# Performance work log

Hardware: AMD Instinct MI355X
Metric: run time of the kernel (lower is better)

The kernel has to match this reference:

```python
import jax, jax.numpy as jnp
import numpy as np

B, N, T, D = 8, 512, 64, 128
H = 8
DK = D // H
KS = 3
CAUSAL_PAD = KS - 1          # query conv: pad both sides, crop tail
SYM_PAD = (KS - 1) // 2      # key conv: 'same' padding


def setup_inputs() -> dict:
    key0 = jax.random.key(0)
    ks = jax.random.split(key0, 12)
    s = 0.05  # weight scale to keep activations in a sane range
    inp = {
        "query": jax.random.normal(ks[0], (B, N, T, D), jnp.float32),
        "key": jax.random.normal(ks[1], (B, N, T, D), jnp.float32),
        "value": jax.random.normal(ks[2], (B, N, T, D), jnp.float32),
        # causal mask (batch, T, T): 1 where attention allowed
        "mask": jnp.broadcast_to(jnp.tril(jnp.ones((T, T), jnp.int32)), (B, T, T)),
        "Wq": jax.random.normal(ks[3], (D, D, 1, KS), jnp.float32) * s,
        "bq": jax.random.normal(ks[4], (D,), jnp.float32) * s,
        "Wk": jax.random.normal(ks[5], (D, D, 1, KS), jnp.float32) * s,
        "bk": jax.random.normal(ks[6], (D,), jnp.float32) * s,
        "W0": jax.random.normal(ks[7], (D, D), jnp.float32) * s,
        "b0": jax.random.normal(ks[8], (D,), jnp.float32) * s,
        "W1": jax.random.normal(ks[9], (D, D), jnp.float32) * s,
        "b1": jax.random.normal(ks[10], (D,), jnp.float32) * s,
        "query_multi_segment": 0,
        "key_multi_segment": 1,
    }
    return inp


def _temporal_conv(x, W, b, pad):
    # x: (B, N, T, D) -> NCHW (B, D, N, T); W: (O, I, 1, K) OIHW
    xt = jnp.transpose(x, (0, 3, 1, 2))
    y = jax.lax.conv_general_dilated(
        xt, W, window_strides=(1, 1),
        padding=[(0, 0), (pad, pad)],
        dimension_numbers=("NCHW", "OIHW", "NCHW"))
    return y + b[None, :, None, None]  # (B, D, N, T')


def _to_heads(y_bdnt, nbatches):
    # (B, D, N, T) -> view (B, H, DK, N, T) -> permute -> (B, N, H, T, DK)
    Bb, Dd, Nn, Tt = y_bdnt.shape
    y = y_bdnt.reshape(Bb, H, DK, Nn, Tt)
    return jnp.transpose(y, (0, 3, 1, 4, 2))


def reference(query, key, value, mask, Wq, bq, Wk, bk, W0, b0, W1, b1,
              query_multi_segment, key_multi_segment):
    del query_multi_segment, key_multi_segment  # static: (False, True) branch, h_length == T
    nbatches = query.shape[0]

    # causal conv for query: pad (k-1) both sides, crop last (k-1)
    q = _temporal_conv(query, Wq, bq, CAUSAL_PAD)[:, :, :, :-CAUSAL_PAD]
    q = _to_heads(q, nbatches)                       # (B, N, H, T, DK)
    # 'same' conv for key
    k = _to_heads(_temporal_conv(key, Wk, bk, SYM_PAD), nbatches)  # (B, N, H, T, DK)

    # value linear: x @ W0.T + b0, then split heads
    v = jnp.einsum("bntd,ed->bnte", value, W0) + b0
    v = jnp.transpose(v.reshape(nbatches, N, T, H, DK), (0, 1, 3, 2, 4))  # (B, N, H, T, DK)

    scores = jnp.einsum("bnhqd,bnhkd->bnhqk", q, k) / jnp.sqrt(jnp.float32(DK))
    m = mask[:, None, None, :, :]                    # (B, 1, 1, T, T)
    scores = jnp.where(m == 0, jnp.float32(-1e9), scores)
    p_attn = jax.nn.softmax(scores, axis=-1)         # dropout p=0.0 -> identity

    x = jnp.einsum("bnhqk,bnhkd->bnhqd", p_attn, v)  # (B, N, H, T, DK)
    x = jnp.transpose(x, (0, 1, 3, 2, 4)).reshape(nbatches, N, T, H * DK)
    return jnp.einsum("bntd,ed->bnte", x, W1) + b1
```

## Files before the change

kernel.cpp:

```cpp
#include <hip/hip_runtime.h>
#include <hip/hip_bf16.h>
#include <stdint.h>
#include <math.h>

constexpr int Tt = 64;
constexpr int Dd = 128;
constexpr int BN = 4096;

typedef short s16x8 __attribute__((ext_vector_type(8)));
typedef short s16x4 __attribute__((ext_vector_type(4)));
typedef float f32x4 __attribute__((ext_vector_type(4)));

__device__ __forceinline__ short f2bf(float f) {
  return (short)__bfloat16_as_ushort(__float2bfloat16(f));
}

#define SQ_OFF   0
#define SK_OFF   16384
#define SV_OFF   32768
#define LDS_TOTAL 49152

__device__ __forceinline__ int swz256(int row, int colElem) {
  return (row << 8) + ((colElem << 1) ^ ((row & 7) << 4));
}
__device__ __forceinline__ int swz128(int row, int colElem) {
  return (row << 7) + ((colElem << 1) ^ ((row & 7) << 4));
}

__global__ void prep_weights(const float* __restrict__ Wq, const float* __restrict__ Wk,
                             const float* __restrict__ W0, const float* __restrict__ W1,
                             short* __restrict__ ws) {
  int i = blockIdx.x * 256 + threadIdx.x;
  if (i >= 131072) return;
  if (i < 49152) {
    int s = i >> 14, rem = i & 16383, o = rem >> 7, ii = rem & 127;
    ws[i] = f2bf(Wq[(o * 128 + ii) * 3 + s] * 0.36067376022224085f);
  } else if (i < 98304) {
    int j = i - 49152;
    int s = j >> 14, rem = j & 16383, o = rem >> 7, ii = rem & 127;
    ws[i] = f2bf(Wk[(o * 128 + ii) * 3 + s]);
  } else if (i < 114688) {
    ws[i] = f2bf(W0[i - 98304]);
  } else {
    ws[i] = f2bf(W1[i - 114688]);
  }
}

__launch_bounds__(512, 4)
__global__ void fused_attn(const float* __restrict__ query, const float* __restrict__ key,
                           const float* __restrict__ value, const short* __restrict__ wsb,
                           const float* __restrict__ bq, const float* __restrict__ bk,
                           const float* __restrict__ b0, const float* __restrict__ b1,
                           float* __restrict__ out) {
  __shared__ unsigned char smem[LDS_TOTAL];
  const int bn = blockIdx.x;
  const int tid = threadIdx.x;
  const int wave = tid >> 6;
  const int lane = tid & 63;
  const size_t base = (size_t)bn * (Tt * Dd);

  const int col = wave * 16 + (lane & 15);
  const int ke = 8 * (lane >> 4);
  const int arow = lane & 15;

  const short* wq = wsb;
  const short* wk = wsb + 49152;
  const short* wv = wsb + 98304;
  const short* w1 = wsb + 114688;

  {
    const int row0 = tid >> 5;
    const int c4 = (tid & 31) << 2;
#pragma unroll
    for (int t3 = 0; t3 < 3; ++t3) {
      const float* sp = (t3 == 0) ? query : (t3 == 1) ? key : value;
      const float4* s4 = (const float4*)(sp + base) + tid;
      const int a0 = ((t3 == 0) ? SQ_OFF : (t3 == 1) ? SK_OFF : SV_OFF) + swz256(row0, c4);
#pragma unroll
      for (int j = 0; j < 4; ++j) {
        float4 v = s4[j * 512];
        s16x4 b = {f2bf(v.x), f2bf(v.y), f2bf(v.z), f2bf(v.w)};
        *(s16x4*)(smem + a0 + j * 4096) = b;
      }
    }
  }
  const float bqv = bq[col] * 0.36067376022224085f;
  const float bkv = bk[col];
  const float b0v = b0[col];
  __syncthreads();

  f32x4 aq[4], ak[4], av[4];
#pragma unroll
  for (int rb = 0; rb < 4; ++rb) {
    aq[rb] = (f32x4){bqv, bqv, bqv, bqv};
    ak[rb] = (f32x4){bkv, bkv, bkv, bkv};
    av[rb] = (f32x4){b0v, b0v, b0v, b0v};
  }
#pragma unroll
  for (int kk = 0; kk < 4; ++kk) {
    s16x8 bvf = *(const s16x8*)(wv + (col << 7) + kk * 32 + ke);
#pragma unroll
    for (int rb = 0; rb < 4; ++rb) {
      s16x8 afv = *(const s16x8*)(smem + SV_OFF + swz256(rb * 16 + arow, kk * 32 + ke));
      av[rb] = __builtin_amdgcn_mfma_f32_16x16x32_bf16(afv, bvf, av[rb], 0, 0, 0);
    }
  }
#pragma unroll
  for (int s = 0; s < 3; ++s) {
#pragma unroll
    for (int kk = 0; kk < 4; ++kk) {
      s16x8 bqf = *(const s16x8*)(wq + (s << 14) + (col << 7) + kk * 32 + ke);
      s16x8 bkf = *(const s16x8*)(wk + (s << 14) + (col << 7) + kk * 32 + ke);
#pragma unroll
      for (int rb = 0; rb < 4; ++rb) {
        const int trq = rb * 16 + arow + s - 2;
        s16x8 afq = (s16x8){0, 0, 0, 0, 0, 0, 0, 0};
        if (rb == 0 && s < 2) {
          if (trq >= 0) afq = *(const s16x8*)(smem + SQ_OFF + swz256(trq, kk * 32 + ke));
        } else {
          afq = *(const s16x8*)(smem + SQ_OFF + swz256(trq, kk * 32 + ke));
        }
        aq[rb] = __builtin_amdgcn_mfma_f32_16x16x32_bf16(afq, bqf, aq[rb], 0, 0, 0);
        const int trk = rb * 16 + arow + s - 1;
        s16x8 afk = (s16x8){0, 0, 0, 0, 0, 0, 0, 0};
        if (rb == 0 && s == 0) {
          if (trk >= 0) afk = *(const s16x8*)(smem + SK_OFF + swz256(trk, kk * 32 + ke));
        } else if (rb == 3 && s == 2) {
          if (trk <= 63) afk = *(const s16x8*)(smem + SK_OFF + swz256(trk, kk * 32 + ke));
        } else {
          afk = *(const s16x8*)(smem + SK_OFF + swz256(trk, kk * 32 + ke));
        }
        ak[rb] = __builtin_amdgcn_mfma_f32_16x16x32_bf16(afk, bkf, ak[rb], 0, 0, 0);
      }
    }
  }
  __syncthreads();

#pragma unroll
  for (int rb = 0; rb < 4; ++rb)
#pragma unroll
    for (int r = 0; r < 4; ++r) {
      const int row = rb * 16 + (lane >> 4) * 4 + r;
      *(short*)(smem + SQ_OFF + swz256(row, col)) = f2bf(aq[rb][r]);
      *(short*)(smem + SK_OFF + swz256(row, col)) = f2bf(ak[rb][r]);
      *(short*)(smem + SV_OFF + swz128(col, row)) = f2bf(av[rb][r]);
    }
  __syncthreads();

  {
    const int g = lane >> 4;
    const int qrow = lane & 15;
#pragma unroll
    for (int j = 0; j < 4; ++j) {
      const int h = (wave + j) & 7;
      const int rb = 3 - j;
      s16x8 bfq = *(const s16x8*)(smem + SQ_OFF + swz256(rb * 16 + qrow, h * 16 + ke));
      f32x4 sacc[4];
#pragma unroll
      for (int c = 0; c <= rb; ++c) {
        s16x8 af = (s16x8){0, 0, 0, 0, 0, 0, 0, 0};
        if (lane < 32)
          af = *(const s16x8*)(smem + SK_OFF + swz256(c * 16 + qrow, h * 16 + ke));
        sacc[c] = __builtin_amdgcn_mfma_f32_16x16x32_bf16(
            af, bfq, (f32x4){0.f, 0.f, 0.f, 0.f}, 0, 0, 0);
      }
      float mx = -3.0e38f;
#pragma unroll
      for (int c = 0; c < rb; ++c)
#pragma unroll
        for (int r = 0; r < 4; ++r) mx = fmaxf(mx, sacc[c][r]);
#pragma unroll
      for (int r = 0; r < 4; ++r) {
        float sv = (4 * g + r <= qrow) ? sacc[rb][r] : -3.0e38f;
        sacc[rb][r] = sv;
        mx = fmaxf(mx, sv);
      }
      mx = fmaxf(mx, __shfl_xor(mx, 16));
      mx = fmaxf(mx, __shfl_xor(mx, 32));
      float sm = 0.f;
#pragma unroll
      for (int c = 0; c <= rb; ++c)
#pragma unroll
        for (int r = 0; r < 4; ++r) {
          float e = exp2f(sacc[c][r] - mx);
          sacc[c][r] = e;
          sm += e;
        }
      sm += __shfl_xor(sm, 16);
      sm += __shfl_xor(sm, 32);
      const float inv = 1.0f / sm;
      f32x4 xacc = (f32x4){0.f, 0.f, 0.f, 0.f};
#pragma unroll
      for (int c = 0; c <= rb; ++c) {
        s16x4 pa;
#pragma unroll
        for (int r = 0; r < 4; ++r) pa[r] = f2bf(sacc[c][r] * inv);
        s16x4 vf = *(const s16x4*)(smem + SV_OFF + swz128(h * 16 + qrow, c * 16 + 4 * g));
        xacc = __builtin_amdgcn_mfma_f32_16x16x16bf16_1k(pa, vf, xacc, 0, 0, 0);
      }
#pragma unroll
      for (int r = 0; r < 4; ++r)
        *(short*)(smem + SQ_OFF + swz256(rb * 16 + 4 * g + r, h * 16 + qrow)) = f2bf(xacc[r]);
    }
  }
  const float bv = b1[col];
  __syncthreads();

  {
    f32x4 acc[4];
#pragma unroll
    for (int rb = 0; rb < 4; ++rb) acc[rb] = (f32x4){bv, bv, bv, bv};
#pragma unroll
    for (int kk = 0; kk < 4; ++kk) {
      s16x8 bf = *(const s16x8*)(w1 + (col << 7) + kk * 32 + ke);
#pragma unroll
      for (int rb = 0; rb < 4; ++rb) {
        s16x8 af = *(const s16x8*)(smem + SQ_OFF + swz256(rb * 16 + arow, kk * 32 + ke));
        acc[rb] = __builtin_amdgcn_mfma_f32_16x16x32_bf16(af, bf, acc[rb], 0, 0, 0);
      }
    }
#pragma unroll
    for (int rb = 0; rb < 4; ++rb)
#pragma unroll
      for (int r = 0; r < 4; ++r) {
        const int row = rb * 16 + (lane >> 4) * 4 + r;
        out[base + (size_t)row * Dd + col] = acc[rb][r];
      }
  }
}

extern "C" void kernel_launch(void* const* d_in, const int* in_sizes, int n_in,
                              void* d_out, int out_size, void* d_ws, size_t ws_size,
                              hipStream_t stream) {
  (void)in_sizes; (void)n_in; (void)out_size; (void)ws_size;
  const float* query = (const float*)d_in[0];
  const float* key   = (const float*)d_in[1];
  const float* value = (const float*)d_in[2];
  const float* Wq = (const float*)d_in[4];
  const float* bq = (const float*)d_in[5];
  const float* Wk = (const float*)d_in[6];
  const float* bk = (const float*)d_in[7];
  const float* W0 = (const float*)d_in[8];
  const float* b0 = (const float*)d_in[9];
  const float* W1 = (const float*)d_in[10];
  const float* b1 = (const float*)d_in[11];
  float* out = (float*)d_out;
  short* wsb = (short*)d_ws;

  hipLaunchKernelGGL(prep_weights, dim3(512), dim3(256), 0, stream, Wq, Wk, W0, W1, wsb);
  hipLaunchKernelGGL(fused_attn, dim3(BN), dim3(512), 0, stream,
                     query, key, value, wsb, bq, bk, b0, b1, out);
}
```

Baseline: 210.1 us.

## Swap MFMA operand order so accumulators hold contiguous features for vector stores

The weight and activation operands of the projection and output MFMAs are swapped, so each lane's accumulator holds four consecutive feature columns of one time row. Results can then go to LDS as 8-byte packed stores and to global memory as 16-byte float4 stores, where the old code wrote scattered 2-byte and 4-byte elements. The PV MFMA is also transposed, and softmax normalization moves from every probability to the final output row. Biases are loaded as float4. This changes fragment layouts across several stages, so any indexing mistake would corrupt results, and LDS bank conflicts may shift.

Result: slower. 217.3 us (+3.4%).

```diff
diff --git a/kernel.cpp b/kernel.cpp
--- a/kernel.cpp
+++ b/kernel.cpp
@@ -59,9 +59,10 @@
   const int lane = tid & 63;
   const size_t base = (size_t)bn * (Tt * Dd);
 
-  const int col = wave * 16 + (lane & 15);
+  const int arow = lane & 15;
   const int ke = 8 * (lane >> 4);
-  const int arow = lane & 15;
+  const int d4 = wave * 16 + (lane >> 4) * 4;
+  const int wrow = wave * 16 + arow;
 
   const short* wq = wsb;
   const short* wk = wsb + 49152;
@@ -84,21 +85,22 @@
       }
     }
   }
-  const float bqv = bq[col] * 0.36067376022224085f;
-  const float bkv = bk[col];
-  const float b0v = b0[col];
-  __syncthreads();
-
+  const float4 bq4 = *(const float4*)(bq + d4);
+  const float4 bk4 = *(const float4*)(bk + d4);
+  const float b0v = b0[wave * 16 + arow];
+  __syncthreads();
+
+  constexpr float LS = 0.36067376022224085f;
   f32x4 aq[4], ak[4], av[4];
 #pragma unroll
-  for (int rb = 0; rb < 4; ++rb) {
-    aq[rb] = (f32x4){bqv, bqv, bqv, bqv};
-    ak[rb] = (f32x4){bkv, bkv, bkv, bkv};
-    av[rb] = (f32x4){b0v, b0v, b0v, b0v};
+  for (int tb = 0; tb < 4; ++tb) {
+    aq[tb] = (f32x4){bq4.x * LS, bq4.y * LS, bq4.z * LS, bq4.w * LS};
+    ak[tb] = (f32x4){bk4.x, bk4.y, bk4.z, bk4.w};
+    av[tb] = (f32x4){b0v, b0v, b0v, b0v};
   }
 #pragma unroll
   for (int kk = 0; kk < 4; ++kk) {
-    s16x8 bvf = *(const s16x8*)(wv + (col << 7) + kk * 32 + ke);
+    s16x8 bvf = *(const s16x8*)(wv + (wrow << 7) + kk * 32 + ke);
 #pragma unroll
     for (int rb = 0; rb < 4; ++rb) {
       s16x8 afv = *(const s16x8*)(smem + SV_OFF + swz256(rb * 16 + arow, kk * 32 + ke));
@@ -109,42 +111,43 @@
   for (int s = 0; s < 3; ++s) {
 #pragma unroll
     for (int kk = 0; kk < 4; ++kk) {
-      s16x8 bqf = *(const s16x8*)(wq + (s << 14) + (col << 7) + kk * 32 + ke);
-      s16x8 bkf = *(const s16x8*)(wk + (s << 14) + (col << 7) + kk * 32 + ke);
-#pragma unroll
-      for (int rb = 0; rb < 4; ++rb) {
-        const int trq = rb * 16 + arow + s - 2;
-        s16x8 afq = (s16x8){0, 0, 0, 0, 0, 0, 0, 0};
-        if (rb == 0 && s < 2) {
-          if (trq >= 0) afq = *(const s16x8*)(smem + SQ_OFF + swz256(trq, kk * 32 + ke));
+      s16x8 wqf = *(const s16x8*)(wq + (s << 14) + (wrow << 7) + kk * 32 + ke);
+      s16x8 wkf = *(const s16x8*)(wk + (s << 14) + (wrow << 7) + kk * 32 + ke);
+#pragma unroll
+      for (int tb = 0; tb < 4; ++tb) {
+        const int trq = tb * 16 + arow + s - 2;
+        s16x8 xq = (s16x8){0, 0, 0, 0, 0, 0, 0, 0};
+        if (tb == 0 && s < 2) {
+          if (trq >= 0) xq = *(const s16x8*)(smem + SQ_OFF + swz256(trq, kk * 32 + ke));
         } else {
-          afq = *(const s16x8*)(smem + SQ_OFF + swz256(trq, kk * 32 + ke));
+          xq = *(const s16x8*)(smem + SQ_OFF + swz256(trq, kk * 32 + ke));
         }
-        aq[rb] = __builtin_amdgcn_mfma_f32_16x16x32_bf16(afq, bqf, aq[rb], 0, 0, 0);
-        const int trk = rb * 16 + arow + s - 1;
-        s16x8 afk = (s16x8){0, 0, 0, 0, 0, 0, 0, 0};
-        if (rb == 0 && s == 0) {
-          if (trk >= 0) afk = *(const s16x8*)(smem + SK_OFF + swz256(trk, kk * 32 + ke));
-        } else if (rb == 3 && s == 2) {
-          if (trk <= 63) afk = *(const s16x8*)(smem + SK_OFF + swz256(trk, kk * 32 + ke));
+        aq[tb] = __builtin_amdgcn_mfma_f32_16x16x32_bf16(wqf, xq, aq[tb], 0, 0, 0);
+        const int trk = tb * 16 + arow + s - 1;
+        s16x8 xk = (s16x8){0, 0, 0, 0, 0, 0, 0, 0};
+        if (tb == 0 && s == 0) {
+          if (trk >= 0) xk = *(const s16x8*)(smem + SK_OFF + swz256(trk, kk * 32 + ke));
+        } else if (tb == 3 && s == 2) {
+          if (trk <= 63) xk = *(const s16x8*)(smem + SK_OFF + swz256(trk, kk * 32 + ke));
         } else {
-          afk = *(const s16x8*)(smem + SK_OFF + swz256(trk, kk * 32 + ke));
+          xk = *(const s16x8*)(smem + SK_OFF + swz256(trk, kk * 32 + ke));
         }
-        ak[rb] = __builtin_amdgcn_mfma_f32_16x16x32_bf16(afk, bkf, ak[rb], 0, 0, 0);
-      }
-    }
-  }
-  __syncthreads();
-
-#pragma unroll
-  for (int rb = 0; rb < 4; ++rb)
-#pragma unroll
-    for (int r = 0; r < 4; ++r) {
-      const int row = rb * 16 + (lane >> 4) * 4 + r;
-      *(short*)(smem + SQ_OFF + swz256(row, col)) = f2bf(aq[rb][r]);
-      *(short*)(smem + SK_OFF + swz256(row, col)) = f2bf(ak[rb][r]);
-      *(short*)(smem + SV_OFF + swz128(col, row)) = f2bf(av[rb][r]);
-    }
+        ak[tb] = __builtin_amdgcn_mfma_f32_16x16x32_bf16(wkf, xk, ak[tb], 0, 0, 0);
+      }
+    }
+  }
+  __syncthreads();
+
+#pragma unroll
+  for (int tb = 0; tb < 4; ++tb) {
+    const int t = tb * 16 + arow;
+    s16x4 pq = {f2bf(aq[tb][0]), f2bf(aq[tb][1]), f2bf(aq[tb][2]), f2bf(aq[tb][3])};
+    *(s16x4*)(smem + SQ_OFF + swz256(t, d4)) = pq;
+    s16x4 pk = {f2bf(ak[tb][0]), f2bf(ak[tb][1]), f2bf(ak[tb][2]), f2bf(ak[tb][3])};
+    *(s16x4*)(smem + SK_OFF + swz256(t, d4)) = pk;
+    s16x4 pv = {f2bf(av[tb][0]), f2bf(av[tb][1]), f2bf(av[tb][2]), f2bf(av[tb][3])};
+    *(s16x4*)(smem + SV_OFF + swz128(wave * 16 + arow, tb * 16 + (lane >> 4) * 4)) = pv;
+  }
   __syncthreads();
 
   {
@@ -194,38 +197,36 @@
       for (int c = 0; c <= rb; ++c) {
         s16x4 pa;
 #pragma unroll
-        for (int r = 0; r < 4; ++r) pa[r] = f2bf(sacc[c][r] * inv);
+        for (int r = 0; r < 4; ++r) pa[r] = f2bf(sacc[c][r]);
         s16x4 vf = *(const s16x4*)(smem + SV_OFF + swz128(h * 16 + qrow, c * 16 + 4 * g));
-        xacc = __builtin_amdgcn_mfma_f32_16x16x16bf16_1k(pa, vf, xacc, 0, 0, 0);
-      }
-#pragma unroll
-      for (int r = 0; r < 4; ++r)
-        *(short*)(smem + SQ_OFF + swz256(rb * 16 + 4 * g + r, h * 16 + qrow)) = f2bf(xacc[r]);
-    }
-  }
-  const float bv = b1[col];
+        xacc = __builtin_amdgcn_mfma_f32_16x16x16bf16_1k(vf, pa, xacc, 0, 0, 0);
+      }
+      s16x4 px = {f2bf(xacc[0] * inv), f2bf(xacc[1] * inv),
+                  f2bf(xacc[2] * inv), f2bf(xacc[3] * inv)};
+      *(s16x4*)(smem + SQ_OFF + swz256(rb * 16 + qrow, h * 16 + 4 * g)) = px;
+    }
+  }
+  const float4 b14 = *(const float4*)(b1 + d4);
   __syncthreads();
 
   {
-    f32x4 acc[4];
-#pragma unroll
-    for (int rb = 0; rb < 4; ++rb) acc[rb] = (f32x4){bv, bv, bv, bv};
+    f32x4 oacc[4];
+#pragma unroll
+    for (int tb = 0; tb < 4; ++tb) oacc[tb] = (f32x4){b14.x, b14.y, b14.z, b14.w};
 #pragma unroll
     for (int kk = 0; kk < 4; ++kk) {
-      s16x8 bf = *(const s16x8*)(w1 + (col << 7) + kk * 32 + ke);
-#pragma unroll
-      for (int rb = 0; rb < 4; ++rb) {
-        s16x8 af = *(const s16x8*)(smem + SQ_OFF + swz256(rb * 16 + arow, kk * 32 + ke));
-        acc[rb] = __builtin_amdgcn_mfma_f32_16x16x32_bf16(af, bf, acc[rb], 0, 0, 0);
-      }
-    }
-#pragma unroll
-    for (int rb = 0; rb < 4; ++rb)
-#pragma unroll
-      for (int r = 0; r < 4; ++r) {
-        const int row = rb * 16 + (lane >> 4) * 4 + r;
-        out[base + (size_t)row * Dd + col] = acc[rb][r];
-      }
+      s16x8 w1f = *(const s16x8*)(w1 + (wrow << 7) + kk * 32 + ke);
+#pragma unroll
+      for (int tb = 0; tb < 4; ++tb) {
+        s16x8 xf = *(const s16x8*)(smem + SQ_OFF + swz256(tb * 16 + arow, kk * 32 + ke));
+        oacc[tb] = __builtin_amdgcn_mfma_f32_16x16x32_bf16(w1f, xf, oacc[tb], 0, 0, 0);
+      }
+    }
+#pragma unroll
+    for (int tb = 0; tb < 4; ++tb) {
+      const int t = tb * 16 + arow;
+      *(f32x4*)(out + base + (size_t)t * Dd + d4) = oacc[tb];
+    }
   }
 }
 
```
